# Performance work log

Hardware: AMD Instinct MI355X
Metric: run time of the kernel (lower is better)

Reference implementation:

```python
import jax, jax.numpy as jnp
import numpy as np

B, S, D, H = 2, 2048, 1024, 16
HD = D // H


def setup_inputs() -> dict:
    key = jax.random.key(0)
    ks = jax.random.split(key, 6)
    sc = 0.02
    return {
        "hidden_states": jax.random.normal(ks[0], (B, S, D), dtype=jnp.float32),
        "attention_mask": jnp.ones((B, S), dtype=bool),
        "Wq": jax.random.normal(ks[1], (D, D), dtype=jnp.float32) * sc,
        "Wk": jax.random.normal(ks[2], (D, D), dtype=jnp.float32) * sc,
        "Wv": jax.random.normal(ks[3], (D, D), dtype=jnp.float32) * sc,
        "Wo": jax.random.normal(ks[4], (D, D), dtype=jnp.float32) * sc,
        "bo": jnp.zeros((D,), dtype=jnp.float32),
    }


def reference(hidden_states, attention_mask, Wq, Wk, Wv, Wo, bo):
    b, s, d_model = hidden_states.shape

    def split_heads(x):  # [B,S,D] -> [B,H,S,hd]
        return x.reshape(b, s, H, HD).transpose(0, 2, 1, 3)

    # nn.Linear applies x @ W.T (bias=False for q/k/v)
    q = split_heads(hidden_states @ Wq.T)
    k = split_heads(hidden_states @ Wk.T)
    v = split_heads(hidden_states @ Wv.T)

    # NOTE: original module does NOT scale by 1/sqrt(d_head)
    score = jnp.einsum("bhqd,bhkd->bhqk", q, k)

    m = attention_mask.astype(bool)
    causal = jnp.tril(jnp.ones((s, s), dtype=bool))  # diagonal=0
    ext_mask = m[:, None, None, :] & m[:, None, :, None] & causal[None, None, :, :]

    lv = jnp.finfo(score.dtype).min
    score = score + lv * (~ext_mask)
    proba = jax.nn.softmax(score, axis=-1)

    context = jnp.einsum("bhqk,bhkd->bhqd", proba, v)
    context = context.transpose(0, 2, 1, 3).reshape(b, s, d_model)
    # VariationalNormalEpanechnikovDropout is identity in eval mode
    output = context @ Wo.T + bo
    return (output, proba)
```

## Files before the change

kernel.cpp:

```cpp
#include <hip/hip_runtime.h>
#include <cstddef>
#include <cstdint>

#define D_MODEL 1024
#define SEQ     2048
#define NHEAD   16
#define HDIM    64
#define BATCH   2
#define M_ROWS  (BATCH * SEQ)

typedef _Float16 f16;
typedef f16   v8h __attribute__((ext_vector_type(8)));
typedef short v8s __attribute__((ext_vector_type(8)));
typedef float v4f __attribute__((ext_vector_type(4)));
typedef unsigned short ushort_t;
typedef unsigned int   uint_t;

__device__ __forceinline__ ushort_t f2h(float x) {
    f16 h = (f16)x;
    return __builtin_bit_cast(ushort_t, h);
}

__device__ __forceinline__ void gl_lds16(const ushort_t* g, ushort_t* l) {
    __builtin_amdgcn_global_load_lds((const __attribute__((address_space(1))) void*)g,
                                     (__attribute__((address_space(3))) void*)l, 16, 0, 0);
}

__global__ __launch_bounds__(256) void convert_all(
    const float* __restrict__ X,  ushort_t* __restrict__ Xh,
    const float* __restrict__ Wq, ushort_t* __restrict__ Wqh,
    const float* __restrict__ Wk, ushort_t* __restrict__ Wkh,
    const float* __restrict__ Wv, ushort_t* __restrict__ Wvh,
    const float* __restrict__ Wo, ushort_t* __restrict__ Woh)
{
    const int blk = blockIdx.x;
    const float* in; ushort_t* hi; int off;
    if (blk < 2048)      { in = X;  hi = Xh;  off = blk; }
    else if (blk < 2560) { in = Wq; hi = Wqh; off = blk - 2048; }
    else if (blk < 3072) { in = Wk; hi = Wkh; off = blk - 2560; }
    else if (blk < 3584) { in = Wv; hi = Wvh; off = blk - 3072; }
    else                 { in = Wo; hi = Woh; off = blk - 3584; }

    const int i = (off * 256 + threadIdx.x) * 8;
    const float4 a = *(const float4*)(in + i);
    const float4 b = *(const float4*)(in + i + 4);
    float x[8] = {a.x, a.y, a.z, a.w, b.x, b.y, b.z, b.w};
    ushort_t h[8];
    #pragma unroll
    for (int j = 0; j < 8; ++j) h[j] = f2h(x[j]);
    *(v8s*)(hi + i) = *(v8s*)h;
}

__global__ __launch_bounds__(256) void gemm_qkv(
    const ushort_t* __restrict__ Xh,
    const ushort_t* __restrict__ Wqh,
    const ushort_t* __restrict__ Wkh,
    const ushort_t* __restrict__ Wvh,
    ushort_t* __restrict__ Qhf,
    ushort_t* __restrict__ Khf,
    ushort_t* __restrict__ Vt)
{
    __shared__ __align__(16) ushort_t Ah[128 * 32];
    __shared__ __align__(16) ushort_t Wh[128 * 32];

    const int z = blockIdx.z;
    const ushort_t* Ag = (z == 2) ? Wvh : Xh;
    const ushort_t* Wg = (z == 2) ? Xh : (z == 1 ? Wkh : Wqh);
    const int m0 = (z == 2) ? (int)blockIdx.y * 128 : (int)blockIdx.x * 128;
    const int n0 = (z == 2) ? (int)blockIdx.x * 128 : (int)blockIdx.y * 128;

    const int tid  = threadIdx.x;
    const int lane = tid & 63, w = tid >> 6;
    const int quad = lane >> 4, l16 = lane & 15;
    const int wr = (w & 1) * 64, wc = (w >> 1) * 64;
    const int srow = lane >> 2, sseg = (lane & 3) * 8;

    v4f acc[4][4];
    #pragma unroll
    for (int i = 0; i < 4; ++i)
        #pragma unroll
        for (int j = 0; j < 4; ++j)
            acc[i][j] = (v4f){0.f, 0.f, 0.f, 0.f};

    for (int k0 = 0; k0 < D_MODEL; k0 += 32) {
        __syncthreads();
        #pragma unroll
        for (int cc = 0; cc < 2; ++cc) {
            const int c = 2 * w + cc;
            gl_lds16(Ag + (size_t)(m0 + c * 16 + srow) * D_MODEL + k0 + sseg, &Ah[c * 512]);
            gl_lds16(Wg + (size_t)(n0 + c * 16 + srow) * D_MODEL + k0 + sseg, &Wh[c * 512]);
        }
        __syncthreads();

        v8h af[4];
        #pragma unroll
        for (int rb = 0; rb < 4; ++rb)
            af[rb] = *(const v8h*)&Ah[(wr + rb*16 + l16) * 32 + quad * 8];
        #pragma unroll
        for (int cb = 0; cb < 4; ++cb) {
            const v8h wf = *(const v8h*)&Wh[(wc + cb*16 + l16) * 32 + quad * 8];
            #pragma unroll
            for (int rb = 0; rb < 4; ++rb)
                acc[rb][cb] = __builtin_amdgcn_mfma_f32_16x16x32_f16(af[rb], wf, acc[rb][cb], 0, 0, 0);
        }
    }

    ushort_t* outp = (z == 2) ? Vt : (z == 1 ? Khf : Qhf);
    #pragma unroll
    for (int rb = 0; rb < 4; ++rb)
        #pragma unroll
        for (int cb = 0; cb < 4; ++cb)
            #pragma unroll
            for (int reg = 0; reg < 4; ++reg) {
                const int m = m0 + wr + rb*16 + quad*4 + reg;
                const int n = n0 + wc + cb*16 + l16;
                const ushort_t hv = f2h(acc[rb][cb][reg]);
                if (z < 2) {
                    const int b = m >> 11, s = m & (SEQ - 1);
                    const int h = n >> 6,  d = n & 63;
                    outp[((size_t)(b*NHEAD + h) * SEQ + s) * HDIM + d] = hv;
                } else {
                    const int h = m >> 6,  dd = m & 63;
                    const int b = n >> 11, s  = n & (SEQ - 1);
                    const size_t idx = (((size_t)(b*NHEAD + h) * (SEQ/64) + (s >> 6)) * HDIM + dd) * 64 + (s & 63);
                    outp[idx] = hv;
                }
            }
}

__global__ __launch_bounds__(256) void gemm_out(
    const ushort_t* __restrict__ Ag,
    const ushort_t* __restrict__ Wg,
    const float* __restrict__ bias,
    float* __restrict__ out)
{
    __shared__ __align__(16) ushort_t Ah[128 * 32];
    __shared__ __align__(16) ushort_t Wh[128 * 32];

    const int tid  = threadIdx.x;
    const int lane = tid & 63, w = tid >> 6;
    const int quad = lane >> 4, l16 = lane & 15;
    const int wr = (w & 1) * 64, wc = (w >> 1) * 64;
    const int m0 = blockIdx.x * 128, n0 = blockIdx.y * 128;
    const int srow = lane >> 2, sseg = (lane & 3) * 8;

    v4f acc[4][4];
    #pragma unroll
    for (int i = 0; i < 4; ++i)
        #pragma unroll
        for (int j = 0; j < 4; ++j)
            acc[i][j] = (v4f){0.f, 0.f, 0.f, 0.f};

    for (int k0 = 0; k0 < D_MODEL; k0 += 32) {
        __syncthreads();
        #pragma unroll
        for (int cc = 0; cc < 2; ++cc) {
            const int c = 2 * w + cc;
            gl_lds16(Ag + (size_t)(m0 + c * 16 + srow) * D_MODEL + k0 + sseg, &Ah[c * 512]);
            gl_lds16(Wg + (size_t)(n0 + c * 16 + srow) * D_MODEL + k0 + sseg, &Wh[c * 512]);
        }
        __syncthreads();

        v8h af[4];
        #pragma unroll
        for (int rb = 0; rb < 4; ++rb)
            af[rb] = *(const v8h*)&Ah[(wr + rb*16 + l16) * 32 + quad * 8];
        #pragma unroll
        for (int cb = 0; cb < 4; ++cb) {
            const v8h wf = *(const v8h*)&Wh[(wc + cb*16 + l16) * 32 + quad * 8];
            #pragma unroll
            for (int rb = 0; rb < 4; ++rb)
                acc[rb][cb] = __builtin_amdgcn_mfma_f32_16x16x32_f16(af[rb], wf, acc[rb][cb], 0, 0, 0);
        }
    }

    #pragma unroll
    for (int rb = 0; rb < 4; ++rb)
        #pragma unroll
        for (int cb = 0; cb < 4; ++cb)
            #pragma unroll
            for (int reg = 0; reg < 4; ++reg) {
                const int m = m0 + wr + rb*16 + quad*4 + reg;
                const int n = n0 + wc + cb*16 + l16;
                out[(size_t)m * D_MODEL + n] = acc[rb][cb][reg] + bias[n];
            }
}

__global__ __launch_bounds__(256) void attn(const ushort_t* __restrict__ Qh,
                                            const ushort_t* __restrict__ Kh,
                                            const ushort_t* __restrict__ Vt,
                                            float* __restrict__ proba,
                                            ushort_t* __restrict__ ctx)
{
    __shared__ __align__(16) ushort_t SM[2 * 8192];
    __shared__ __align__(16) ushort_t Pbuf[4][16 * 72];

    const int tid  = threadIdx.x;
    const int lane = tid & 63, w = tid >> 6;
    const int quad = lane >> 4, l16 = lane & 15;
    const int qt = (int)gridDim.x - 1 - (int)blockIdx.x;
    const int bh = blockIdx.y;
    const int r0 = qt * 128;
    const int NT = 2 * qt + 2;
    const size_t base = (size_t)bh * SEQ * HDIM;

    v8h qf[4];
    #pragma unroll
    for (int f = 0; f < 2; ++f) {
        const ushort_t* qp = Qh + base + (size_t)(r0 + f*64 + w*16 + l16) * HDIM + quad*8;
        qf[2*f]   = *(const v8h*)qp;
        qf[2*f+1] = *(const v8h*)(qp + 32);
    }

    const int krow = lane >> 3;
    const int ksrc = krow * 64 + (((lane & 7) ^ krow) * 8);

    #define STAGE_K128(kt, bb) do { \
        const ushort_t* g = Kh + base + (size_t)(kt) * 8192; \
        ushort_t* d = SM + (bb) * 8192; \
        _Pragma("unroll") \
        for (int c = 0; c < 4; ++c) \
            gl_lds16(g + (4*w+c)*512 + ksrc, d + (4*w+c)*512); \
    } while (0)

    #define STAGE_K64(kt, bb) do { \
        const ushort_t* g = Kh + base + (size_t)(kt) * 4096; \
        ushort_t* d = SM + (bb) * 8192; \
        gl_lds16(g + (2*w)  *512 + ksrc, d + (2*w)  *512); \
        gl_lds16(g + (2*w+1)*512 + ksrc, d + (2*w+1)*512); \
    } while (0)

    #define STAGE_V64(kt, bb) do { \
        const ushort_t* g = Vt + ((size_t)bh * (SEQ/64) + (kt)) * 4096; \
        ushort_t* d = SM + (bb) * 8192 + 4096; \
        gl_lds16(g + (2*w)  *512 + ksrc, d + (2*w)  *512); \
        gl_lds16(g + (2*w+1)*512 + ksrc, d + (2*w+1)*512); \
    } while (0)

    const int sw = quad ^ (l16 & 7);

    #define SCORE_P(KB, s, f) do { \
        _Pragma("unroll") \
        for (int cb = 0; cb < 4; ++cb) { \
            const ushort_t* kr = (KB) + (cb*16 + l16) * 64; \
            const v8h kh0 = *(const v8h*)(kr + sw*8); \
            const v8h kh1 = *(const v8h*)(kr + (sw^4)*8); \
            v4f s0 = (v4f){0.f, 0.f, 0.f, 0.f}; \
            s0 = __builtin_amdgcn_mfma_f32_16x16x32_f16(qf[2*(f)],   kh0, s0, 0, 0, 0); \
            s0 = __builtin_amdgcn_mfma_f32_16x16x32_f16(qf[2*(f)+1], kh1, s0, 0, 0, 0); \
            (s)[cb] = s0; \
        } \
    } while (0)

    float l_run[2][4];
    #pragma unroll
    for (int f = 0; f < 2; ++f)
        #pragma unroll
        for (int i = 0; i < 4; ++i) l_run[f][i] = 0.f;

    STAGE_K128(0, 0);
    __syncthreads();
    int buf = 0;
    for (int kt = 0; kt <= qt; ++kt) {
        if (kt < qt) STAGE_K128(kt + 1, buf ^ 1);
        const ushort_t* KB = SM + buf * 8192;
        #pragma unroll
        for (int f = 0; f < 2; ++f)
            #pragma unroll
            for (int hh = 0; hh < 2; ++hh) {
                v4f s[4];
                SCORE_P(KB + hh * 4096, s, f);
                #pragma unroll
                for (int reg = 0; reg < 4; ++reg) {
                    const int rowg = r0 + f*64 + w*16 + quad*4 + reg;
                    float ps = 0.f;
                    #pragma unroll
                    for (int cb = 0; cb < 4; ++cb) {
                        const int col = kt*128 + hh*64 + cb*16 + l16;
                        ps += (col <= rowg) ? __expf(s[cb][reg]) : 0.f;
                    }
                    l_run[f][reg] += ps;
                }
            }
        __syncthreads();
        buf ^= 1;
    }

    float rli[2][4];
    #pragma unroll
    for (int f = 0; f < 2; ++f)
        #pragma unroll
        for (int reg = 0; reg < 4; ++reg) {
            float l = l_run[f][reg];
            #pragma unroll
            for (int d = 1; d < 16; d <<= 1) l += __shfl_xor(l, d);
            rli[f][reg] = 1.0f / l;
        }

    v4f oacc[8];
    #pragma unroll
    for (int i = 0; i < 8; ++i) oacc[i] = (v4f){0.f, 0.f, 0.f, 0.f};

    float* prow = proba + (size_t)bh * SEQ * SEQ;
    ushort_t* pb = Pbuf[w];

    STAGE_K64(0, 0);
    STAGE_V64(0, 0);
    __syncthreads();
    buf = 0;
    for (int kt = 0; kt < NT; ++kt) {
        if (kt + 1 < NT) { STAGE_K64(kt + 1, buf ^ 1); STAGE_V64(kt + 1, buf ^ 1); }
        const ushort_t* KB = SM + buf * 8192;
        const ushort_t* VB = KB + 4096;
        #pragma unroll
        for (int f = 0; f < 2; ++f) {
            v4f s[4];
            SCORE_P(KB, s, f);
            #pragma unroll
            for (int cb = 0; cb < 4; ++cb) {
                const int col = kt*64 + cb*16 + l16;
                #pragma unroll
                for (int reg = 0; reg < 4; ++reg) {
                    const int rowg = r0 + f*64 + w*16 + quad*4 + reg;
                    const float p = (col <= rowg) ? __expf(s[cb][reg]) * rli[f][reg] : 0.f;
                    prow[(size_t)rowg * SEQ + col] = p;
                    pb[(quad*4 + reg)*72 + cb*16 + l16] = f2h(p);
                }
            }
            const v8h pf0 = *(const v8h*)&pb[l16*72 + quad*8];
            const v8h pf1 = *(const v8h*)&pb[l16*72 + 32 + quad*8];
            #pragma unroll
            for (int nb = 0; nb < 4; ++nb) {
                const ushort_t* vr = VB + (nb*16 + l16) * 64;
                const v8h vf0 = *(const v8h*)(vr + sw*8);
                const v8h vf1 = *(const v8h*)(vr + (sw^4)*8);
                oacc[f*4+nb] = __builtin_amdgcn_mfma_f32_16x16x32_f16(pf0, vf0, oacc[f*4+nb], 0, 0, 0);
                oacc[f*4+nb] = __builtin_amdgcn_mfma_f32_16x16x32_f16(pf1, vf1, oacc[f*4+nb], 0, 0, 0);
            }
        }
        __syncthreads();
        buf ^= 1;
    }

    for (int c0 = NT * 64; c0 < SEQ; c0 += 64) {
        const float4 z = {0.f, 0.f, 0.f, 0.f};
        #pragma unroll
        for (int f = 0; f < 2; ++f) {
            float* zp = prow + (size_t)(r0 + f*64 + w*16 + l16) * SEQ + c0 + quad*16;
            #pragma unroll
            for (int i = 0; i < 4; ++i) *(float4*)(zp + i*4) = z;
        }
    }

    const int b = bh >> 4, h = bh & 15;
    #pragma unroll
    for (int f = 0; f < 2; ++f)
        #pragma unroll
        for (int nb = 0; nb < 4; ++nb)
            #pragma unroll
            for (int reg = 0; reg < 4; ++reg) {
                const int rowg = r0 + f*64 + w*16 + quad*4 + reg;
                ctx[(size_t)(b*SEQ + rowg) * D_MODEL + h*HDIM + nb*16 + l16] = f2h(oacc[f*4+nb][reg]);
            }
    #undef STAGE_K128
    #undef STAGE_K64
    #undef STAGE_V64
    #undef SCORE_P
}

extern "C" void kernel_launch(void* const* d_in, const int* in_sizes, int n_in,
                              void* d_out, int out_size, void* d_ws, size_t ws_size,
                              hipStream_t stream)
{
    (void)in_sizes; (void)n_in; (void)out_size; (void)ws_size;
    const float* X  = (const float*)d_in[0];
    const float* Wq = (const float*)d_in[2];
    const float* Wk = (const float*)d_in[3];
    const float* Wv = (const float*)d_in[4];
    const float* Wo = (const float*)d_in[5];
    const float* bo = (const float*)d_in[6];

    float* out   = (float*)d_out;
    float* proba = out + (size_t)M_ROWS * D_MODEL;

    const size_t QE = (size_t)BATCH * NHEAD * SEQ * HDIM;
    const size_t WE = (size_t)D_MODEL * D_MODEL;

    ushort_t* wsu  = (ushort_t*)d_ws;
    ushort_t* Qhf  = wsu;
    ushort_t* Khf  = wsu + QE;
    ushort_t* Vt   = wsu + 2*QE;
    ushort_t* ctxb = wsu + 3*QE;
    ushort_t* Woh  = wsu + 4*QE;

    ushort_t* s2  = (ushort_t*)proba;
    ushort_t* Xh  = s2;
    ushort_t* Wqh = s2 + QE;
    ushort_t* Wkh = Wqh + WE;
    ushort_t* Wvh = Wkh + WE;

    convert_all<<<4096, 256, 0, stream>>>(X, Xh, Wq, Wqh, Wk, Wkh,
                                          Wv, Wvh, Wo, Woh);

    gemm_qkv<<<dim3(M_ROWS/128, D_MODEL/128, 3), 256, 0, stream>>>(
        Xh, Wqh, Wkh, Wvh, Qhf, Khf, Vt);

    attn<<<dim3(SEQ/128, BATCH*NHEAD), 256, 0, stream>>>(Qhf, Khf, Vt, proba, ctxb);

    gemm_out<<<dim3(M_ROWS/128, D_MODEL/128), 256, 0, stream>>>(
        ctxb, Woh, bo, out);
}
```

Baseline: 703.8 us.

## Use nontemporal stores, remap attention blocks, and raise MFMA wave priority

Stores for the probability matrix, the zero-fill region and the output projection become nontemporal, so the large write stream does not pollute the cache. The zero-fill loop is restructured so each wave writes whole rows contiguously. Attention blocks are remapped so groups of eight heads sharing a query tile launch together, and s_setprio raises wave priority around the MFMA sections. These target the write bandwidth of the large proba output and scheduling balance. The new grid mapping assumes a fixed grid shape (16 tiles by 32 heads).

```diff
diff --git a/kernel.cpp b/kernel.cpp
--- a/kernel.cpp
+++ b/kernel.cpp
@@ -182,7 +182,8 @@
             for (int reg = 0; reg < 4; ++reg) {
                 const int m = m0 + wr + rb*16 + quad*4 + reg;
                 const int n = n0 + wc + cb*16 + l16;
-                out[(size_t)m * D_MODEL + n] = acc[rb][cb][reg] + bias[n];
+                __builtin_nontemporal_store(acc[rb][cb][reg] + bias[n],
+                                            &out[(size_t)m * D_MODEL + n]);
             }
 }
 
@@ -198,8 +199,12 @@
     const int tid  = threadIdx.x;
     const int lane = tid & 63, w = tid >> 6;
     const int quad = lane >> 4, l16 = lane & 15;
-    const int qt = (int)gridDim.x - 1 - (int)blockIdx.x;
-    const int bh = blockIdx.y;
+
+    const int d   = (int)(blockIdx.x + gridDim.x * blockIdx.y);
+    const int grp = d >> 3;
+    const int bh  = (d & 7) + 8 * (grp >> 4);
+    const int qt  = 15 - (grp & 15);
+
     const int r0 = qt * 128;
     const int NT = 2 * qt + 2;
     const size_t base = (size_t)bh * SEQ * HDIM;
@@ -217,29 +222,30 @@
 
     #define STAGE_K128(kt, bb) do { \
         const ushort_t* g = Kh + base + (size_t)(kt) * 8192; \
-        ushort_t* d = SM + (bb) * 8192; \
+        ushort_t* dst = SM + (bb) * 8192; \
         _Pragma("unroll") \
         for (int c = 0; c < 4; ++c) \
-            gl_lds16(g + (4*w+c)*512 + ksrc, d + (4*w+c)*512); \
+            gl_lds16(g + (4*w+c)*512 + ksrc, dst + (4*w+c)*512); \
     } while (0)
 
     #define STAGE_K64(kt, bb) do { \
         const ushort_t* g = Kh + base + (size_t)(kt) * 4096; \
-        ushort_t* d = SM + (bb) * 8192; \
-        gl_lds16(g + (2*w)  *512 + ksrc, d + (2*w)  *512); \
-        gl_lds16(g + (2*w+1)*512 + ksrc, d + (2*w+1)*512); \
+        ushort_t* dst = SM + (bb) * 8192; \
+        gl_lds16(g + (2*w)  *512 + ksrc, dst + (2*w)  *512); \
+        gl_lds16(g + (2*w+1)*512 + ksrc, dst + (2*w+1)*512); \
     } while (0)
 
     #define STAGE_V64(kt, bb) do { \
         const ushort_t* g = Vt + ((size_t)bh * (SEQ/64) + (kt)) * 4096; \
-        ushort_t* d = SM + (bb) * 8192 + 4096; \
-        gl_lds16(g + (2*w)  *512 + ksrc, d + (2*w)  *512); \
-        gl_lds16(g + (2*w+1)*512 + ksrc, d + (2*w+1)*512); \
+        ushort_t* dst = SM + (bb) * 8192 + 4096; \
+        gl_lds16(g + (2*w)  *512 + ksrc, dst + (2*w)  *512); \
+        gl_lds16(g + (2*w+1)*512 + ksrc, dst + (2*w+1)*512); \
     } while (0)
 
     const int sw = quad ^ (l16 & 7);
 
     #define SCORE_P(KB, s, f) do { \
+        __builtin_amdgcn_s_setprio(1); \
         _Pragma("unroll") \
         for (int cb = 0; cb < 4; ++cb) { \
             const ushort_t* kr = (KB) + (cb*16 + l16) * 64; \
@@ -250,6 +256,7 @@
             s0 = __builtin_amdgcn_mfma_f32_16x16x32_f16(qf[2*(f)+1], kh1, s0, 0, 0, 0); \
             (s)[cb] = s0; \
         } \
+        __builtin_amdgcn_s_setprio(0); \
     } while (0)
 
     float l_run[2][4];
@@ -293,7 +300,7 @@
         for (int reg = 0; reg < 4; ++reg) {
             float l = l_run[f][reg];
             #pragma unroll
-            for (int d = 1; d < 16; d <<= 1) l += __shfl_xor(l, d);
+            for (int dd = 1; dd < 16; dd <<= 1) l += __shfl_xor(l, dd);
             rli[f][reg] = 1.0f / l;
         }
 
@@ -323,12 +330,13 @@
                 for (int reg = 0; reg < 4; ++reg) {
                     const int rowg = r0 + f*64 + w*16 + quad*4 + reg;
                     const float p = (col <= rowg) ? __expf(s[cb][reg]) * rli[f][reg] : 0.f;
-                    prow[(size_t)rowg * SEQ + col] = p;
+                    __builtin_nontemporal_store(p, &prow[(size_t)rowg * SEQ + col]);
                     pb[(quad*4 + reg)*72 + cb*16 + l16] = f2h(p);
                 }
             }
             const v8h pf0 = *(const v8h*)&pb[l16*72 + quad*8];
             const v8h pf1 = *(const v8h*)&pb[l16*72 + 32 + quad*8];
+            __builtin_amdgcn_s_setprio(1);
             #pragma unroll
             for (int nb = 0; nb < 4; ++nb) {
                 const ushort_t* vr = VB + (nb*16 + l16) * 64;
@@ -337,18 +345,19 @@
                 oacc[f*4+nb] = __builtin_amdgcn_mfma_f32_16x16x32_f16(pf0, vf0, oacc[f*4+nb], 0, 0, 0);
                 oacc[f*4+nb] = __builtin_amdgcn_mfma_f32_16x16x32_f16(pf1, vf1, oacc[f*4+nb], 0, 0, 0);
             }
+            __builtin_amdgcn_s_setprio(0);
         }
         __syncthreads();
         buf ^= 1;
     }
 
-    for (int c0 = NT * 64; c0 < SEQ; c0 += 64) {
-        const float4 z = {0.f, 0.f, 0.f, 0.f};
-        #pragma unroll
-        for (int f = 0; f < 2; ++f) {
-            float* zp = prow + (size_t)(r0 + f*64 + w*16 + l16) * SEQ + c0 + quad*16;
-            #pragma unroll
-            for (int i = 0; i < 4; ++i) *(float4*)(zp + i*4) = z;
+    {
+        const int cstart = NT * 64;
+        const v4f z = (v4f){0.f, 0.f, 0.f, 0.f};
+        for (int rr = 0; rr < 32; ++rr) {
+            float* zp = prow + (size_t)(r0 + w*32 + rr) * SEQ;
+            for (int c = cstart + lane*4; c < SEQ; c += 256)
+                __builtin_nontemporal_store(z, (v4f*)(zp + c));
         }
     }
 
```

Measured after the change: 731.9 us. +4.0%, slower.
